# Optimization experiments

Measured on AMD Instinct MI355X. Metric: run time of the kernel, lower is better.

The kernel has to match this reference:

```python
import jax, jax.numpy as jnp
import numpy as np

N = 1048576          # query points
L = 16               # hash levels per encoding
T = 524288           # 2**19 hashmap entries per level
F = 2                # features per level
BASE = 16.0
GROWTH = 1.3819      # per_level_scale so level 15 ~ 2048
RES = np.asarray(BASE * GROWTH ** np.arange(L), dtype=np.float32)
PRIME0 = np.uint32(1)
PRIME1 = np.uint32(2654435761)


def hashgrid_encode(points, table):
    """points: [N,2] in [0,1); table: [L,T,F] -> [N, L*F]."""
    def level(tab, res):
        pos = points * res                      # [N,2]
        pf = jnp.floor(pos)
        w = pos - pf                            # bilinear weights [N,2]
        pi = pf.astype(jnp.int32)

        def corner(dx, dy):
            c = (pi + jnp.array([dx, dy], jnp.int32)).astype(jnp.uint32)
            h = (c[:, 0] * PRIME0) ^ (c[:, 1] * PRIME1)
            return tab[(h % jnp.uint32(T)).astype(jnp.int32)]  # [N,F]

        wx, wy = w[:, 0:1], w[:, 1:2]
        return (corner(0, 0) * (1 - wx) * (1 - wy)
                + corner(1, 0) * wx * (1 - wy)
                + corner(0, 1) * (1 - wx) * wy
                + corner(1, 1) * wx * wy)       # [N,F]

    feats = jax.vmap(level)(table, jnp.asarray(RES))   # [L,N,F]
    return jnp.transpose(feats, (1, 0, 2)).reshape(points.shape[0], L * F)


def setup_inputs() -> dict:
    key = jax.random.key(0)
    ks = jax.random.split(key, 10)
    pts = {name: jax.random.uniform(ks[i], (N, 2), dtype=jnp.float32)
           for i, name in enumerate(
               ['points_xy', 'points_xz', 'points_yz', 'points_xt', 'points_yt', 'points_zt'])}
    tables = (jax.random.uniform(ks[6], (6, L, T, F), dtype=jnp.float32) * 2e-4 - 1e-4)
    d_in = 6 * L * F + 6 * 2   # 204
    W1 = jax.random.normal(ks[7], (d_in, 64), dtype=jnp.float32) / np.float32(np.sqrt(d_in))
    W2 = jax.random.normal(ks[8], (64, 64), dtype=jnp.float32) / np.float32(8.0)
    W3 = jax.random.normal(ks[9], (64, 3), dtype=jnp.float32) / np.float32(8.0)
    return {**pts, 'tables': tables, 'W1': W1, 'W2': W2, 'W3': W3}


def reference(points_xy, points_xz, points_yz, points_xt, points_yt, points_zt,
              tables, W1, W2, W3):
    pts = [points_xy, points_xz, points_yz, points_xt, points_yt, points_zt]
    parts = []
    for i in range(6):                       # fixed structural loop over 6 planes
        parts.append(hashgrid_encode(pts[i], tables[i]))
        parts.append(pts[i])
    enc = jnp.concatenate(parts, axis=-1)    # [N, 204]
    h = jax.nn.relu(enc @ W1)
    h = jax.nn.relu(h @ W2)
    return h @ W3                            # [N, 3]
```

## Files before the change

### kernel.cpp

```cpp
#include <hip/hip_runtime.h>

#define THREADS 256
#define LVLS 16
#define TSZ 524288u
#define TMASK 524287u
#define PRIME1 2654435761u
#define HID 64
#define NBIN 16384
#define ENC_STRIDE 104
#define MLP_TILES 8

typedef __attribute__((ext_vector_type(8))) short bf16x8;
typedef __attribute__((ext_vector_type(4))) float f32x4;

constexpr float resf(int l) { double r = 16.0; for (int i = 0; i < l; ++i) r *= 1.3819; return (float)r; }

__device__ __constant__ float c_RES[LVLS] = {
    resf(0),  resf(1),  resf(2),  resf(3),
    resf(4),  resf(5),  resf(6),  resf(7),
    resf(8),  resf(9),  resf(10), resf(11),
    resf(12), resf(13), resf(14), resf(15)
};

__device__ __forceinline__ unsigned packbf2(float a, float b) {
    unsigned ua = __float_as_uint(a), ub = __float_as_uint(b);
    ua += 0x7FFFu + ((ua >> 16) & 1u);
    ub += 0x7FFFu + ((ub >> 16) & 1u);
    return (ua >> 16) | (ub & 0xFFFF0000u);
}

__device__ __forceinline__ unsigned short bf16rne(float f) {
    unsigned u = __float_as_uint(f);
    u += 0x7FFFu + ((u >> 16) & 1u);
    return (unsigned short)(u >> 16);
}

__device__ __forceinline__ unsigned part1by1(unsigned v) {
    v &= 0xFFu;
    v = (v | (v << 4)) & 0x0F0Fu;
    v = (v | (v << 2)) & 0x3333u;
    v = (v | (v << 1)) & 0x5555u;
    return v;
}

__device__ __forceinline__ float2 load_pt(int s, int i,
    const float* pxy, const float* pxz, const float* pyz,
    const float* pxt, const float* pyt, const float* pzt)
{
    switch (s) {
        case 0: return ((const float2*)pxy)[i];
        case 1: return ((const float2*)pxz)[i];
        case 2: return ((const float2*)pyz)[i];
        case 3: return ((const float2*)pxt)[i];
        case 4: return ((const float2*)pyt)[i];
        default: return ((const float2*)pzt)[i];
    }
}

__device__ __forceinline__ unsigned bin_key(float2 pt) {
    const int xb = min(127, (int)(pt.x * 128.f));
    const int yb = min(127, (int)(pt.y * 128.f));
    return part1by1((unsigned)xb) | (part1by1((unsigned)yb) << 1);
}

__global__ __launch_bounds__(256) void pack_w1_k(const float* __restrict__ W1,
                                                 unsigned short* __restrict__ W1B)
{
    const int e = blockIdx.x * 256 + threadIdx.x;
    if (e >= 7 * 4 * 64 * 8) return;
    const int j = e & 7;
    const int lane = (e >> 3) & 63;
    const int n = (e >> 9) & 3;
    const int t = e >> 11;
    const int k = t * 32 + ((lane >> 4) << 3) + j;
    const int col = n * 16 + (lane & 15);
    float v = 0.f;
    if (k < 192) { const int s = k >> 5, rem = k & 31; v = W1[(s * 34 + rem) * HID + col]; }
    else if (k < 204) { const int q = k - 192; v = W1[((q >> 1) * 34 + 32 + (q & 1)) * HID + col]; }
    W1B[e] = bf16rne(v);
}

__global__ __launch_bounds__(256) void pack_w2_k(const float* __restrict__ W2,
                                                 unsigned short* __restrict__ W2B)
{
    const int e = blockIdx.x * 256 + threadIdx.x;
    if (e >= 2 * 4 * 64 * 8) return;
    const int j = e & 7;
    const int lane = (e >> 3) & 63;
    const int n = (e >> 9) & 3;
    const int t = e >> 11;
    const int k = t * 32 + ((lane >> 4) << 3) + j;
    const int col = n * 16 + (lane & 15);
    W2B[e] = bf16rne(W2[k * HID + col]);
}

__global__ void zero_hist_k(int* __restrict__ hist) {
    const int i = blockIdx.x * blockDim.x + threadIdx.x;
    if (i < 6 * NBIN) hist[i] = 0;
}

__global__ __launch_bounds__(THREADS) void hist_k(
    const float* __restrict__ pxy, const float* __restrict__ pxz,
    const float* __restrict__ pyz, const float* __restrict__ pxt,
    const float* __restrict__ pyt, const float* __restrict__ pzt,
    int* __restrict__ hist, unsigned short* __restrict__ keys, int npts, int bpp)
{
    const int s = blockIdx.x / bpp;
    const int i = (blockIdx.x - s * bpp) * THREADS + threadIdx.x;
    if (i >= npts) return;
    const float2 pt = load_pt(s, i, pxy, pxz, pyz, pxt, pyt, pzt);
    const unsigned key = bin_key(pt);
    keys[(size_t)s * npts + i] = (unsigned short)key;
    atomicAdd(&hist[s * NBIN + key], 1);
}

__global__ __launch_bounds__(1024) void scan_k(int* __restrict__ hist)
{
    __shared__ int sb[1024];
    const int p = blockIdx.x;
    const int t = threadIdx.x;
    const int base = p * NBIN + t * 16;
    int h[16], pre[16];
    int run = 0;
    #pragma unroll
    for (int i = 0; i < 16; ++i) { h[i] = hist[base + i]; pre[i] = run; run += h[i]; }
    sb[t] = run;
    __syncthreads();
    for (int off = 1; off < 1024; off <<= 1) {
        const int v = (t >= off) ? sb[t - off] : 0;
        __syncthreads();
        sb[t] += v;
        __syncthreads();
    }
    const int start = sb[t] - run;
    #pragma unroll
    for (int i = 0; i < 16; ++i) hist[base + i] = start + pre[i];
}

__global__ __launch_bounds__(THREADS) void scatter_k(
    const unsigned short* __restrict__ keys, int* __restrict__ curs,
    int* __restrict__ sidx, int npts, int bpp)
{
    const int s = blockIdx.x / bpp;
    const int i = (blockIdx.x - s * bpp) * THREADS + threadIdx.x;
    if (i >= npts) return;
    const unsigned key = keys[(size_t)s * npts + i];
    const int pos = atomicAdd(&curs[s * NBIN + key], 1);
    sidx[(size_t)s * npts + pos] = i;
}

__global__ __launch_bounds__(THREADS, 6) void gather_sorted_k(
    const float* __restrict__ pxy, const float* __restrict__ pxz,
    const float* __restrict__ pyz, const float* __restrict__ pxt,
    const float* __restrict__ pyt, const float* __restrict__ pzt,
    const float* __restrict__ tables, const int* __restrict__ sidx,
    unsigned* __restrict__ encW, int npts, int bpp)
{
    int bid = blockIdx.x;
    const int G = gridDim.x;
    if ((G & 7) == 0) {
        const int chunk = G >> 3;
        bid = (bid & 7) * chunk + (bid >> 3);
    }
    const int s = bid / bpp;
    const int i = (bid - s * bpp) * THREADS + threadIdx.x;
    if (i >= npts) return;

    const int orig = sidx[(size_t)s * npts + i];
    const float2 pt = load_pt(s, orig, pxy, pxz, pyz, pxt, pyt, pzt);
    const float2* tbase = ((const float2*)tables) + (size_t)s * LVLS * TSZ;

    unsigned ew[LVLS];
    #pragma unroll
    for (int l = 0; l < LVLS; ++l) {
        const float r = c_RES[l];
        const float fx = pt.x * r, fy = pt.y * r;
        const float flx = floorf(fx), fly = floorf(fy);
        const float wx = fx - flx, wy = fy - fly;
        const unsigned x0 = (unsigned)(int)flx;
        const unsigned y0 = (unsigned)(int)fly;
        const unsigned hy0 = y0 * PRIME1;
        const unsigned hy1 = hy0 + PRIME1;
        const float2* tab = tbase + (size_t)l * TSZ;
        const float2 f00 = tab[(x0 ^ hy0) & TMASK];
        const float2 f10 = tab[((x0 + 1u) ^ hy0) & TMASK];
        const float2 f01 = tab[(x0 ^ hy1) & TMASK];
        const float2 f11 = tab[((x0 + 1u) ^ hy1) & TMASK];
        const float w00 = (1.f - wx) * (1.f - wy);
        const float w10 = wx * (1.f - wy);
        const float w01 = (1.f - wx) * wy;
        const float w11 = wx * wy;
        const float e0 = f00.x * w00 + f10.x * w10 + f01.x * w01 + f11.x * w11;
        const float e1 = f00.y * w00 + f10.y * w10 + f01.y * w01 + f11.y * w11;
        ew[l] = packbf2(e0, e1);
    }

    unsigned* rowp = encW + (size_t)orig * ENC_STRIDE;
    uint4* dst = (uint4*)(rowp + s * LVLS);
    dst[0] = make_uint4(ew[0],  ew[1],  ew[2],  ew[3]);
    dst[1] = make_uint4(ew[4],  ew[5],  ew[6],  ew[7]);
    dst[2] = make_uint4(ew[8],  ew[9],  ew[10], ew[11]);
    dst[3] = make_uint4(ew[12], ew[13], ew[14], ew[15]);
    rowp[96 + s] = packbf2(pt.x, pt.y);
    if (s == 0) { rowp[102] = 0u; rowp[103] = 0u; }
}

__global__ __launch_bounds__(256, 2) void mlp_mfma_k(
    const unsigned* __restrict__ encW, const unsigned short* __restrict__ W1Bg,
    const unsigned short* __restrict__ W2Bg, const float* __restrict__ W3,
    float* __restrict__ out, int npts)
{
    __shared__ uint4 sW1B[1792];
    __shared__ uint4 sW2B[512];
    __shared__ float sW3[192];
    __shared__ unsigned short sH1[4][1024];

    const int tid = threadIdx.x;
    for (int i = tid; i < 1792; i += 256) sW1B[i] = ((const uint4*)W1Bg)[i];
    for (int i = tid; i < 512; i += 256) sW2B[i] = ((const uint4*)W2Bg)[i];
    for (int i = tid; i < 192; i += 256) sW3[i] = W3[i];
    __syncthreads();

    const int w = tid >> 6, lane = tid & 63;
    const int row = lane & 15, g = lane >> 4;
    const int blk0 = blockIdx.x * (64 * MLP_TILES);

    for (int it = 0; it < MLP_TILES; ++it) {
        const int p0 = blk0 + (it * 4 + w) * 16;
        if (p0 + 16 > npts) { __syncthreads(); __syncthreads(); continue; }

        f32x4 acc0 = {0.f,0.f,0.f,0.f}, acc1 = acc0, acc2_ = acc0, acc3 = acc0;
        const unsigned* arow = encW + (size_t)(p0 + row) * ENC_STRIDE;
        #pragma unroll
        for (int t = 0; t < 7; ++t) {
            const int gw = (t == 6) ? (g & 1) : g;
            const uint4 av = *(const uint4*)(arow + t * 16 + gw * 4);
            const bf16x8 a = *(const bf16x8*)&av;
            acc0 = __builtin_amdgcn_mfma_f32_16x16x32_bf16(a, *(const bf16x8*)&sW1B[(t*4+0)*64 + lane], acc0, 0, 0, 0);
            acc1 = __builtin_amdgcn_mfma_f32_16x16x32_bf16(a, *(const bf16x8*)&sW1B[(t*4+1)*64 + lane], acc1, 0, 0, 0);
            acc2_ = __builtin_amdgcn_mfma_f32_16x16x32_bf16(a, *(const bf16x8*)&sW1B[(t*4+2)*64 + lane], acc2_, 0, 0, 0);
            acc3 = __builtin_amdgcn_mfma_f32_16x16x32_bf16(a, *(const bf16x8*)&sW1B[(t*4+3)*64 + lane], acc3, 0, 0, 0);
        }

        #pragma unroll
        for (int r = 0; r < 4; ++r) {
            const int rr = g * 4 + r;
            const int base = rr * 64;
            const int swz = (rr & 7) << 3;
            sH1[w][(base + 0 * 16 + row) ^ swz] = bf16rne(fmaxf(acc0[r], 0.f));
            sH1[w][(base + 1 * 16 + row) ^ swz] = bf16rne(fmaxf(acc1[r], 0.f));
            sH1[w][(base + 2 * 16 + row) ^ swz] = bf16rne(fmaxf(acc2_[r], 0.f));
            sH1[w][(base + 3 * 16 + row) ^ swz] = bf16rne(fmaxf(acc3[r], 0.f));
        }
        __syncthreads();

        f32x4 b0 = {0.f,0.f,0.f,0.f}, b1 = b0, b2 = b0, b3 = b0;
        #pragma unroll
        for (int t = 0; t < 2; ++t) {
            const int kidx = (row * 64 + t * 32 + g * 8) ^ ((row & 7) << 3);
            const bf16x8 a2 = *(const bf16x8*)&sH1[w][kidx];
            b0 = __builtin_amdgcn_mfma_f32_16x16x32_bf16(a2, *(const bf16x8*)&sW2B[(t*4+0)*64 + lane], b0, 0, 0, 0);
            b1 = __builtin_amdgcn_mfma_f32_16x16x32_bf16(a2, *(const bf16x8*)&sW2B[(t*4+1)*64 + lane], b1, 0, 0, 0);
            b2 = __builtin_amdgcn_mfma_f32_16x16x32_bf16(a2, *(const bf16x8*)&sW2B[(t*4+2)*64 + lane], b2, 0, 0, 0);
            b3 = __builtin_amdgcn_mfma_f32_16x16x32_bf16(a2, *(const bf16x8*)&sW2B[(t*4+3)*64 + lane], b3, 0, 0, 0);
        }

        float o[4][3];
        #pragma unroll
        for (int r = 0; r < 4; ++r) { o[r][0] = 0.f; o[r][1] = 0.f; o[r][2] = 0.f; }
        #pragma unroll
        for (int n = 0; n < 4; ++n) {
            const int m = n * 16 + row;
            const float w30 = sW3[m * 3 + 0], w31 = sW3[m * 3 + 1], w32 = sW3[m * 3 + 2];
            const f32x4 bb = (n == 0) ? b0 : (n == 1) ? b1 : (n == 2) ? b2 : b3;
            #pragma unroll
            for (int r = 0; r < 4; ++r) {
                const float h = fmaxf(bb[r], 0.f);
                o[r][0] += h * w30; o[r][1] += h * w31; o[r][2] += h * w32;
            }
        }
        #pragma unroll
        for (int m = 1; m < 16; m <<= 1) {
            #pragma unroll
            for (int r = 0; r < 4; ++r) {
                o[r][0] += __shfl_xor(o[r][0], m, 64);
                o[r][1] += __shfl_xor(o[r][1], m, 64);
                o[r][2] += __shfl_xor(o[r][2], m, 64);
            }
        }
        if (row == 0) {
            #pragma unroll
            for (int r = 0; r < 4; ++r) {
                const int p = p0 + g * 4 + r;
                out[p * 3 + 0] = o[r][0];
                out[p * 3 + 1] = o[r][1];
                out[p * 3 + 2] = o[r][2];
            }
        }
        __syncthreads();
    }
}

__global__ __launch_bounds__(THREADS, 4) void fused_mono(
    const float* __restrict__ pxy, const float* __restrict__ pxz,
    const float* __restrict__ pyz, const float* __restrict__ pxt,
    const float* __restrict__ pyt, const float* __restrict__ pzt,
    const float* __restrict__ tables, const float* __restrict__ W1,
    const float* __restrict__ W2, const float* __restrict__ W3,
    float* __restrict__ out, int npts)
{
    const int gid = blockIdx.x * THREADS + threadIdx.x;

    float h1[HID];
    #pragma unroll
    for (int k = 0; k < HID; ++k) h1[k] = 0.f;

    #pragma unroll 1
    for (int s = 0; s < 6; ++s) {
        const float2 pt = load_pt(s, gid, pxy, pxz, pyz, pxt, pyt, pzt);
        const float px = pt.x, py = pt.y;
        const float2* tbase = ((const float2*)tables) + (size_t)s * LVLS * TSZ;
        const float* w1s = W1 + (s * 34) * HID;

        #pragma unroll 2
        for (int l = 0; l < LVLS; ++l) {
            const float r = c_RES[l];
            const float fx = px * r, fy = py * r;
            const float flx = floorf(fx), fly = floorf(fy);
            const float wx = fx - flx, wy = fy - fly;
            const unsigned x0 = (unsigned)(int)flx;
            const unsigned y0 = (unsigned)(int)fly;
            const unsigned hy0 = y0 * PRIME1;
            const unsigned hy1 = hy0 + PRIME1;
            const float2* tab = tbase + (size_t)l * TSZ;
            const float2 f00 = tab[(x0 ^ hy0) & TMASK];
            const float2 f10 = tab[((x0 + 1u) ^ hy0) & TMASK];
            const float2 f01 = tab[(x0 ^ hy1) & TMASK];
            const float2 f11 = tab[((x0 + 1u) ^ hy1) & TMASK];
            const float w00 = (1.f - wx) * (1.f - wy);
            const float w10 = wx * (1.f - wy);
            const float w01 = (1.f - wx) * wy;
            const float w11 = wx * wy;
            const float e0 = f00.x * w00 + f10.x * w10 + f01.x * w01 + f11.x * w11;
            const float e1 = f00.y * w00 + f10.y * w10 + f01.y * w01 + f11.y * w11;
            const float4* wa = (const float4*)(w1s + (2 * l) * HID);
            const float4* wb = wa + 16;
            #pragma unroll
            for (int q = 0; q < 16; ++q) {
                const float4 a = wa[q];
                const float4 b = wb[q];
                h1[4*q+0] += e0 * a.x + e1 * b.x;
                h1[4*q+1] += e0 * a.y + e1 * b.y;
                h1[4*q+2] += e0 * a.z + e1 * b.z;
                h1[4*q+3] += e0 * a.w + e1 * b.w;
            }
        }
        const float4* wa = (const float4*)(w1s + 32 * HID);
        const float4* wb = wa + 16;
        #pragma unroll
        for (int q = 0; q < 16; ++q) {
            const float4 a = wa[q];
            const float4 b = wb[q];
            h1[4*q+0] += px * a.x + py * b.x;
            h1[4*q+1] += px * a.y + py * b.y;
            h1[4*q+2] += px * a.z + py * b.z;
            h1[4*q+3] += px * a.w + py * b.w;
        }
    }

    #pragma unroll
    for (int k = 0; k < HID; ++k) h1[k] = fmaxf(h1[k], 0.f);

    float o0 = 0.f, o1 = 0.f, o2 = 0.f;
    #pragma unroll 1
    for (int c = 0; c < 4; ++c) {
        float t[16];
        #pragma unroll
        for (int i = 0; i < 16; ++i) t[i] = 0.f;
        #pragma unroll
        for (int k = 0; k < HID; ++k) {
            const float4* w2r = (const float4*)(W2 + k * HID + c * 16);
            const float hk = h1[k];
            const float4 a = w2r[0];
            const float4 b = w2r[1];
            const float4 d = w2r[2];
            const float4 e = w2r[3];
            t[0]  += hk * a.x;  t[1]  += hk * a.y;  t[2]  += hk * a.z;  t[3]  += hk * a.w;
            t[4]  += hk * b.x;  t[5]  += hk * b.y;  t[6]  += hk * b.z;  t[7]  += hk * b.w;
            t[8]  += hk * d.x;  t[9]  += hk * d.y;  t[10] += hk * d.z;  t[11] += hk * d.w;
            t[12] += hk * e.x;  t[13] += hk * e.y;  t[14] += hk * e.z;  t[15] += hk * e.w;
        }
        #pragma unroll
        for (int i = 0; i < 16; ++i) {
            const float tt = fmaxf(t[i], 0.f);
            const int m = c * 16 + i;
            o0 += tt * W3[m * 3 + 0];
            o1 += tt * W3[m * 3 + 1];
            o2 += tt * W3[m * 3 + 2];
        }
    }

    if (gid < npts) {
        out[3 * gid + 0] = o0;
        out[3 * gid + 1] = o1;
        out[3 * gid + 2] = o2;
    }
}

extern "C" void kernel_launch(void* const* d_in, const int* in_sizes, int n_in,
                              void* d_out, int out_size, void* d_ws, size_t ws_size,
                              hipStream_t stream)
{
    const float* pxy = (const float*)d_in[0];
    const float* pxz = (const float*)d_in[1];
    const float* pyz = (const float*)d_in[2];
    const float* pxt = (const float*)d_in[3];
    const float* pyt = (const float*)d_in[4];
    const float* pzt = (const float*)d_in[5];
    const float* tables = (const float*)d_in[6];
    const float* W1 = (const float*)d_in[7];
    const float* W2 = (const float*)d_in[8];
    const float* W3 = (const float*)d_in[9];
    float* out = (float*)d_out;

    const int npts = in_sizes[0] / 2;
    const int bpp = (npts + THREADS - 1) / THREADS;

    const size_t off_w1b  = 0;
    const size_t off_w2b  = 28672;
    const size_t off_sidx = 65536;
    size_t off_enc = off_sidx + (size_t)6 * npts * 4;
    off_enc = (off_enc + 127) & ~(size_t)127;
    const size_t need = off_enc + (size_t)npts * ENC_STRIDE * 4;

    if (ws_size >= need && (npts % (64 * MLP_TILES)) == 0 && npts % THREADS == 0) {
        char* ws = (char*)d_ws;
        unsigned short* W1B = (unsigned short*)(ws + off_w1b);
        unsigned short* W2B = (unsigned short*)(ws + off_w2b);
        int* sidx = (int*)(ws + off_sidx);
        unsigned* encW = (unsigned*)(ws + off_enc);
        unsigned short* keys = (unsigned short*)encW;
        int* hist = (int*)((char*)encW + (size_t)6 * npts * 2);

        hipLaunchKernelGGL(zero_hist_k, dim3((6 * NBIN + THREADS - 1) / THREADS),
                           dim3(THREADS), 0, stream, hist);
        hipLaunchKernelGGL(hist_k, dim3(6 * bpp), dim3(THREADS), 0, stream,
                           pxy, pxz, pyz, pxt, pyt, pzt, hist, keys, npts, bpp);
        hipLaunchKernelGGL(scan_k, dim3(6), dim3(1024), 0, stream, hist);
        hipLaunchKernelGGL(pack_w1_k, dim3(56), dim3(256), 0, stream, W1, W1B);
        hipLaunchKernelGGL(pack_w2_k, dim3(16), dim3(256), 0, stream, W2, W2B);
        hipLaunchKernelGGL(scatter_k, dim3(6 * bpp), dim3(THREADS), 0, stream,
                           keys, hist, sidx, npts, bpp);
        hipLaunchKernelGGL(gather_sorted_k, dim3(6 * bpp), dim3(THREADS), 0, stream,
                           pxy, pxz, pyz, pxt, pyt, pzt, tables, sidx, encW, npts, bpp);
        hipLaunchKernelGGL(mlp_mfma_k, dim3(npts / (64 * MLP_TILES)), dim3(256), 0, stream,
                           encW, W1B, W2B, W3, out, npts);
    } else {
        hipLaunchKernelGGL(fused_mono, dim3(bpp), dim3(THREADS), 0, stream,
                           pxy, pxz, pyz, pxt, pyt, pzt, tables, W1, W2, W3, out, npts);
    }
}
```

Baseline: 1.471 ms.

## Write encodings in sorted order and gather them via inverse permutation in MLP

The gather kernel now writes each plane's 16-word encoding contiguously at its sorted position instead of scattering it into a strided per-point row. The scatter kernel additionally records an inverse permutation, which the MLP kernel uses to gather the six encoding chunks. The MLP kernel also reloads the raw coordinates itself. The table lookups are batched four levels at a time to raise memory-level parallelism, and the gather kernel's launch bound drops from 6 to 5 waves. This turns the gather kernel's scattered writes into coalesced ones. The cost is an extra inverse-index array, and the MLP reads become random 64-byte loads.

Result: faster. 1.255 ms (-14.7%).

```diff
diff --git a/kernel.cpp b/kernel.cpp
--- a/kernel.cpp
+++ b/kernel.cpp
@@ -7,7 +7,6 @@
 #define PRIME1 2654435761u
 #define HID 64
 #define NBIN 16384
-#define ENC_STRIDE 104
 #define MLP_TILES 8
 
 typedef __attribute__((ext_vector_type(8))) short bf16x8;
@@ -139,7 +138,7 @@
 
 __global__ __launch_bounds__(THREADS) void scatter_k(
     const unsigned short* __restrict__ keys, int* __restrict__ curs,
-    int* __restrict__ sidx, int npts, int bpp)
+    int* __restrict__ sidx, int* __restrict__ inv, int npts, int bpp)
 {
     const int s = blockIdx.x / bpp;
     const int i = (blockIdx.x - s * bpp) * THREADS + threadIdx.x;
@@ -147,14 +146,15 @@
     const unsigned key = keys[(size_t)s * npts + i];
     const int pos = atomicAdd(&curs[s * NBIN + key], 1);
     sidx[(size_t)s * npts + pos] = i;
-}
-
-__global__ __launch_bounds__(THREADS, 6) void gather_sorted_k(
+    inv[(size_t)s * npts + i] = pos;
+}
+
+__global__ __launch_bounds__(THREADS, 5) void gather_sorted_k(
     const float* __restrict__ pxy, const float* __restrict__ pxz,
     const float* __restrict__ pyz, const float* __restrict__ pxt,
     const float* __restrict__ pyt, const float* __restrict__ pzt,
     const float* __restrict__ tables, const int* __restrict__ sidx,
-    unsigned* __restrict__ encW, int npts, int bpp)
+    unsigned* __restrict__ encP, int npts, int bpp)
 {
     int bid = blockIdx.x;
     const int G = gridDim.x;
@@ -168,47 +168,57 @@
 
     const int orig = sidx[(size_t)s * npts + i];
     const float2 pt = load_pt(s, orig, pxy, pxz, pyz, pxt, pyt, pzt);
-    const float2* tbase = ((const float2*)tables) + (size_t)s * LVLS * TSZ;
+    const float2* tab0 = ((const float2*)tables) + (size_t)s * LVLS * TSZ;
 
     unsigned ew[LVLS];
     #pragma unroll
-    for (int l = 0; l < LVLS; ++l) {
-        const float r = c_RES[l];
-        const float fx = pt.x * r, fy = pt.y * r;
-        const float flx = floorf(fx), fly = floorf(fy);
-        const float wx = fx - flx, wy = fy - fly;
-        const unsigned x0 = (unsigned)(int)flx;
-        const unsigned y0 = (unsigned)(int)fly;
-        const unsigned hy0 = y0 * PRIME1;
-        const unsigned hy1 = hy0 + PRIME1;
-        const float2* tab = tbase + (size_t)l * TSZ;
-        const float2 f00 = tab[(x0 ^ hy0) & TMASK];
-        const float2 f10 = tab[((x0 + 1u) ^ hy0) & TMASK];
-        const float2 f01 = tab[(x0 ^ hy1) & TMASK];
-        const float2 f11 = tab[((x0 + 1u) ^ hy1) & TMASK];
-        const float w00 = (1.f - wx) * (1.f - wy);
-        const float w10 = wx * (1.f - wy);
-        const float w01 = (1.f - wx) * wy;
-        const float w11 = wx * wy;
-        const float e0 = f00.x * w00 + f10.x * w10 + f01.x * w01 + f11.x * w11;
-        const float e1 = f00.y * w00 + f10.y * w10 + f01.y * w01 + f11.y * w11;
-        ew[l] = packbf2(e0, e1);
-    }
-
-    unsigned* rowp = encW + (size_t)orig * ENC_STRIDE;
-    uint4* dst = (uint4*)(rowp + s * LVLS);
+    for (int g4 = 0; g4 < 4; ++g4) {
+        float2 cor[16];
+        float wxs[4], wys[4];
+        #pragma unroll
+        for (int q = 0; q < 4; ++q) {
+            const int l = g4 * 4 + q;
+            const float r = c_RES[l];
+            const float fx = pt.x * r, fy = pt.y * r;
+            const float flx = floorf(fx), fly = floorf(fy);
+            wxs[q] = fx - flx; wys[q] = fy - fly;
+            const unsigned x0 = (unsigned)(int)flx;
+            const unsigned y0 = (unsigned)(int)fly;
+            const unsigned hy0 = y0 * PRIME1;
+            const unsigned hy1 = hy0 + PRIME1;
+            const float2* tab = tab0 + (size_t)l * TSZ;
+            cor[q * 4 + 0] = tab[(x0 ^ hy0) & TMASK];
+            cor[q * 4 + 1] = tab[((x0 + 1u) ^ hy0) & TMASK];
+            cor[q * 4 + 2] = tab[(x0 ^ hy1) & TMASK];
+            cor[q * 4 + 3] = tab[((x0 + 1u) ^ hy1) & TMASK];
+        }
+        #pragma unroll
+        for (int q = 0; q < 4; ++q) {
+            const float wx = wxs[q], wy = wys[q];
+            const float w00 = (1.f - wx) * (1.f - wy);
+            const float w10 = wx * (1.f - wy);
+            const float w01 = (1.f - wx) * wy;
+            const float w11 = wx * wy;
+            const float e0 = cor[q*4+0].x * w00 + cor[q*4+1].x * w10 + cor[q*4+2].x * w01 + cor[q*4+3].x * w11;
+            const float e1 = cor[q*4+0].y * w00 + cor[q*4+1].y * w10 + cor[q*4+2].y * w01 + cor[q*4+3].y * w11;
+            ew[g4 * 4 + q] = packbf2(e0, e1);
+        }
+    }
+
+    uint4* dst = (uint4*)(encP + ((size_t)s * npts + i) * 16);
     dst[0] = make_uint4(ew[0],  ew[1],  ew[2],  ew[3]);
     dst[1] = make_uint4(ew[4],  ew[5],  ew[6],  ew[7]);
     dst[2] = make_uint4(ew[8],  ew[9],  ew[10], ew[11]);
     dst[3] = make_uint4(ew[12], ew[13], ew[14], ew[15]);
-    rowp[96 + s] = packbf2(pt.x, pt.y);
-    if (s == 0) { rowp[102] = 0u; rowp[103] = 0u; }
 }
 
 __global__ __launch_bounds__(256, 2) void mlp_mfma_k(
-    const unsigned* __restrict__ encW, const unsigned short* __restrict__ W1Bg,
-    const unsigned short* __restrict__ W2Bg, const float* __restrict__ W3,
-    float* __restrict__ out, int npts)
+    const float* __restrict__ pxy, const float* __restrict__ pxz,
+    const float* __restrict__ pyz, const float* __restrict__ pxt,
+    const float* __restrict__ pyt, const float* __restrict__ pzt,
+    const unsigned* __restrict__ encP, const int* __restrict__ inv,
+    const unsigned short* __restrict__ W1Bg, const unsigned short* __restrict__ W2Bg,
+    const float* __restrict__ W3, float* __restrict__ out, int npts)
 {
     __shared__ uint4 sW1B[1792];
     __shared__ uint4 sW2B[512];
@@ -229,17 +239,45 @@
         const int p0 = blk0 + (it * 4 + w) * 16;
         if (p0 + 16 > npts) { __syncthreads(); __syncthreads(); continue; }
 
+        const int p = p0 + row;
+        int ip[6];
+        #pragma unroll
+        for (int t = 0; t < 6; ++t) ip[t] = inv[(size_t)t * npts + p];
+        uint4 av[6];
+        #pragma unroll
+        for (int t = 0; t < 6; ++t)
+            av[t] = *(const uint4*)(encP + ((size_t)t * npts + ip[t]) * 16 + g * 4);
+
+        unsigned cw0 = 0, cw1 = 0, cw2 = 0, cw3 = 0;
+        if (g == 0) {
+            float2 c0 = load_pt(0, p, pxy, pxz, pyz, pxt, pyt, pzt);
+            float2 c1 = load_pt(1, p, pxy, pxz, pyz, pxt, pyt, pzt);
+            float2 c2 = load_pt(2, p, pxy, pxz, pyz, pxt, pyt, pzt);
+            float2 c3 = load_pt(3, p, pxy, pxz, pyz, pxt, pyt, pzt);
+            cw0 = packbf2(c0.x, c0.y); cw1 = packbf2(c1.x, c1.y);
+            cw2 = packbf2(c2.x, c2.y); cw3 = packbf2(c3.x, c3.y);
+        } else if (g == 1) {
+            float2 c4 = load_pt(4, p, pxy, pxz, pyz, pxt, pyt, pzt);
+            float2 c5 = load_pt(5, p, pxy, pxz, pyz, pxt, pyt, pzt);
+            cw0 = packbf2(c4.x, c4.y); cw1 = packbf2(c5.x, c5.y);
+        }
+        const uint4 avc = make_uint4(cw0, cw1, cw2, cw3);
+
         f32x4 acc0 = {0.f,0.f,0.f,0.f}, acc1 = acc0, acc2_ = acc0, acc3 = acc0;
-        const unsigned* arow = encW + (size_t)(p0 + row) * ENC_STRIDE;
-        #pragma unroll
-        for (int t = 0; t < 7; ++t) {
-            const int gw = (t == 6) ? (g & 1) : g;
-            const uint4 av = *(const uint4*)(arow + t * 16 + gw * 4);
-            const bf16x8 a = *(const bf16x8*)&av;
+        #pragma unroll
+        for (int t = 0; t < 6; ++t) {
+            const bf16x8 a = *(const bf16x8*)&av[t];
             acc0 = __builtin_amdgcn_mfma_f32_16x16x32_bf16(a, *(const bf16x8*)&sW1B[(t*4+0)*64 + lane], acc0, 0, 0, 0);
             acc1 = __builtin_amdgcn_mfma_f32_16x16x32_bf16(a, *(const bf16x8*)&sW1B[(t*4+1)*64 + lane], acc1, 0, 0, 0);
             acc2_ = __builtin_amdgcn_mfma_f32_16x16x32_bf16(a, *(const bf16x8*)&sW1B[(t*4+2)*64 + lane], acc2_, 0, 0, 0);
             acc3 = __builtin_amdgcn_mfma_f32_16x16x32_bf16(a, *(const bf16x8*)&sW1B[(t*4+3)*64 + lane], acc3, 0, 0, 0);
+        }
+        {
+            const bf16x8 a = *(const bf16x8*)&avc;
+            acc0 = __builtin_amdgcn_mfma_f32_16x16x32_bf16(a, *(const bf16x8*)&sW1B[(6*4+0)*64 + lane], acc0, 0, 0, 0);
+            acc1 = __builtin_amdgcn_mfma_f32_16x16x32_bf16(a, *(const bf16x8*)&sW1B[(6*4+1)*64 + lane], acc1, 0, 0, 0);
+            acc2_ = __builtin_amdgcn_mfma_f32_16x16x32_bf16(a, *(const bf16x8*)&sW1B[(6*4+2)*64 + lane], acc2_, 0, 0, 0);
+            acc3 = __builtin_amdgcn_mfma_f32_16x16x32_bf16(a, *(const bf16x8*)&sW1B[(6*4+3)*64 + lane], acc3, 0, 0, 0);
         }
 
         #pragma unroll
@@ -291,10 +329,10 @@
         if (row == 0) {
             #pragma unroll
             for (int r = 0; r < 4; ++r) {
-                const int p = p0 + g * 4 + r;
-                out[p * 3 + 0] = o[r][0];
-                out[p * 3 + 1] = o[r][1];
-                out[p * 3 + 2] = o[r][2];
+                const int pp = p0 + g * 4 + r;
+                out[pp * 3 + 0] = o[r][0];
+                out[pp * 3 + 1] = o[r][1];
+                out[pp * 3 + 2] = o[r][2];
             }
         }
         __syncthreads();
@@ -429,18 +467,20 @@
     const size_t off_w1b  = 0;
     const size_t off_w2b  = 28672;
     const size_t off_sidx = 65536;
-    size_t off_enc = off_sidx + (size_t)6 * npts * 4;
+    const size_t off_inv  = off_sidx + (size_t)6 * npts * 4;
+    size_t off_enc = off_inv + (size_t)6 * npts * 4;
     off_enc = (off_enc + 127) & ~(size_t)127;
-    const size_t need = off_enc + (size_t)npts * ENC_STRIDE * 4;
+    const size_t need = off_enc + (size_t)6 * npts * 64;
 
     if (ws_size >= need && (npts % (64 * MLP_TILES)) == 0 && npts % THREADS == 0) {
         char* ws = (char*)d_ws;
         unsigned short* W1B = (unsigned short*)(ws + off_w1b);
         unsigned short* W2B = (unsigned short*)(ws + off_w2b);
         int* sidx = (int*)(ws + off_sidx);
-        unsigned* encW = (unsigned*)(ws + off_enc);
-        unsigned short* keys = (unsigned short*)encW;
-        int* hist = (int*)((char*)encW + (size_t)6 * npts * 2);
+        int* inv  = (int*)(ws + off_inv);
+        unsigned* encP = (unsigned*)(ws + off_enc);
+        unsigned short* keys = (unsigned short*)encP;
+        int* hist = (int*)((char*)encP + (size_t)6 * npts * 2);
 
         hipLaunchKernelGGL(zero_hist_k, dim3((6 * NBIN + THREADS - 1) / THREADS),
                            dim3(THREADS), 0, stream, hist);
@@ -450,11 +490,11 @@
         hipLaunchKernelGGL(pack_w1_k, dim3(56), dim3(256), 0, stream, W1, W1B);
         hipLaunchKernelGGL(pack_w2_k, dim3(16), dim3(256), 0, stream, W2, W2B);
         hipLaunchKernelGGL(scatter_k, dim3(6 * bpp), dim3(THREADS), 0, stream,
-                           keys, hist, sidx, npts, bpp);
+                           keys, hist, sidx, inv, npts, bpp);
         hipLaunchKernelGGL(gather_sorted_k, dim3(6 * bpp), dim3(THREADS), 0, stream,
-                           pxy, pxz, pyz, pxt, pyt, pzt, tables, sidx, encW, npts, bpp);
+                           pxy, pxz, pyz, pxt, pyt, pzt, tables, sidx, encP, npts, bpp);
         hipLaunchKernelGGL(mlp_mfma_k, dim3(npts / (64 * MLP_TILES)), dim3(256), 0, stream,
-                           encW, W1B, W2B, W3, out, npts);
+                           pxy, pxz, pyz, pxt, pyt, pzt, encP, inv, W1B, W2B, W3, out, npts);
     } else {
         hipLaunchKernelGGL(fused_mono, dim3(bpp), dim3(THREADS), 0, stream,
                            pxy, pxz, pyz, pxt, pyt, pzt, tables, W1, W2, W3, out, npts);
```
